# Performance work log

Hardware: AMD Instinct MI355X
Metric: run time of the kernel (lower is better)

Reference implementation:

```python
import jax, jax.numpy as jnp
import numpy as np

N_NODES = 50000


def _gcn_norm(edge_index, num_nodes):
    # PyG GCNConv default: add self-loops, symmetric normalization D^-1/2 A D^-1/2
    row, col = edge_index[0], edge_index[1]
    loop = jnp.arange(num_nodes, dtype=edge_index.dtype)
    row = jnp.concatenate([row, loop])
    col = jnp.concatenate([col, loop])
    deg = jax.ops.segment_sum(jnp.ones_like(col, dtype=jnp.float32), col,
                              num_segments=num_nodes)
    deg_inv_sqrt = jnp.where(deg > 0, jax.lax.rsqrt(deg), 0.0)
    norm = deg_inv_sqrt[row] * deg_inv_sqrt[col]  # [E + N]
    return row, col, norm


def _gcn_conv(x, row, col, norm, W, b):
    h = x @ W                                   # [N, out]
    msg = h[row] * norm[:, None]                # gather + scale, [E+N, out]
    out = jax.ops.segment_sum(msg, col, num_segments=x.shape[0])  # scatter-add
    return out + b


def setup_inputs() -> dict:
    key = jax.random.key(0)
    k_x, k_e, k_w1, k_w2 = jax.random.split(key, 4)
    n, e, d = N_NODES, 800000, 64
    x = jax.random.normal(k_x, (n, d), dtype=jnp.float32)
    edge_index = jax.random.randint(k_e, (2, e), 0, n, dtype=jnp.int64)
    # Glorot init like PyG's Linear inside GCNConv (bias separate, zero-init here as randn-small)
    s1 = (6.0 / (d + d)) ** 0.5
    W1 = jax.random.uniform(k_w1, (d, d), jnp.float32, -s1, s1)
    W2 = jax.random.uniform(k_w2, (d, d), jnp.float32, -s1, s1)
    b1 = jnp.zeros((d,), jnp.float32)
    b2 = jnp.zeros((d,), jnp.float32)
    return {"x": x, "edge_index": edge_index, "W1": W1, "b1": b1, "W2": W2, "b2": b2}


def reference(x, edge_index, W1, b1, W2, b2):
    row, col, norm = _gcn_norm(edge_index, x.shape[0])
    h = _gcn_conv(x, row, col, norm, W1, b1)   # layer 1: in -> out
    h = _gcn_conv(h, row, col, norm, W2, b2)   # layer 2: out -> out
    return h
```

## Files before the change

kernel.cpp:

```cpp
#include <hip/hip_runtime.h>
#include <hip/hip_fp16.h>

#define DD 64
#define BSH 6
#define BNODES 64
#define NSUB 16
#define SCAP 128
#define BCAP 1536

__global__ __launch_bounds__(256) void k_zero(int4* __restrict__ p, int n4) {
    int i = blockIdx.x * 256 + threadIdx.x;
    if (i < n4) p[i] = make_int4(0, 0, 0, 0);
}

__global__ __launch_bounds__(256) void k_fill3(const int* __restrict__ rowi,
                                               const int* __restrict__ coli,
                                               int* __restrict__ cur,
                                               unsigned int* __restrict__ pk, int E) {
    int i = blockIdx.x * 256 + threadIdx.x;
    if (i < E) {
        int c = coli[i];
        int idx = (c >> BSH) * NSUB + (blockIdx.x & (NSUB - 1));
        int p = atomicAdd(&cur[idx * 16], 1);
        if (p < SCAP)
            pk[(size_t)idx * SCAP + p] =
                (unsigned int)rowi[i] | ((unsigned int)(c & (BNODES - 1)) << 16);
    }
}

__global__ __launch_bounds__(256) void k_bsort(const int* __restrict__ cur,
                                               const unsigned int* __restrict__ pk,
                                               int* __restrict__ off_s,
                                               int* __restrict__ off_e,
                                               float* __restrict__ dis,
                                               int* __restrict__ srt, int n) {
    __shared__ unsigned int stage[NSUB * SCAP];
    __shared__ int cnt[BNODES];
    __shared__ int cbase[BNODES];
    __shared__ int sb[NSUB + 1];
    int t = threadIdx.x;
    int b = blockIdx.x;

    if (t < BNODES) cnt[t] = 0;
    if (t < NSUB) {
        int v = cur[(b * NSUB + t) * 16];
        if (v > SCAP) v = SCAP;
        int x = v;
#pragma unroll
        for (int d = 1; d < NSUB; d <<= 1) {
            int u = __shfl_up(x, d, NSUB);
            if ((t & (NSUB - 1)) >= d) x += u;
        }
        sb[t + 1] = x;
        if (t == 0) sb[0] = 0;
    }
    __syncthreads();
    int tot = sb[NSUB];

#pragma unroll
    for (int s = 0; s < NSUB; ++s) {
        int c0 = sb[s], len = sb[s + 1] - c0;
        const unsigned int* src = pk + ((size_t)b * NSUB + s) * SCAP;
        for (int i = t; i < len; i += 256) stage[c0 + i] = src[i];
    }
    __syncthreads();

    for (int i = t; i < tot; i += 256) atomicAdd(&cnt[stage[i] >> 16], 1);
    __syncthreads();

    if (t < BNODES) {
        int v = cnt[t], x = v;
#pragma unroll
        for (int d = 1; d < 64; d <<= 1) {
            int u = __shfl_up(x, d);
            if (t >= d) x += u;
        }
        int excl = x - v;
        cbase[t] = excl;
        int c = b * BNODES + t;
        if (c < n) {
            off_s[c] = b * BCAP + excl;
            off_e[c] = b * BCAP + excl + v;
            dis[c] = rsqrtf((float)(v + 1));
        }
    }
    __syncthreads();

    int sbeg = b * BCAP;
    for (int i = t; i < tot; i += 256) {
        unsigned int k = stage[i];
        int pos = atomicAdd(&cbase[k >> 16], 1);
        srt[sbeg + pos] = (int)(k & 0xFFFFu);
    }
}

__global__ __launch_bounds__(64) void k_mm(const float* __restrict__ X,
                                           const float* __restrict__ W,
                                           const float* __restrict__ dis,
                                           __half* __restrict__ H, int n) {
    int lane  = threadIdx.x;
    int tile  = blockIdx.x >> 1;
    int jbase = (blockIdx.x & 1) * 32;
    int r     = tile * 64 + lane;
    int rc    = min(r, n - 1);

    const float4* X4 = (const float4*)X;
    float acc[32];
#pragma unroll
    for (int j = 0; j < 32; ++j) acc[j] = 0.f;

#pragma unroll 1
    for (int kc = 0; kc < 16; ++kc) {
        float4 xv = X4[(size_t)rc * 16 + kc];
        const float* W0 = W + (kc * 4) * 64 + jbase;
#pragma unroll
        for (int u = 0; u < 4; ++u) {
            float xk = (u == 0) ? xv.x : (u == 1) ? xv.y : (u == 2) ? xv.z : xv.w;
            const float* Wk = W0 + u * 64;
#pragma unroll
            for (int j = 0; j < 32; ++j)
                acc[j] = fmaf(xk, Wk[j], acc[j]);
        }
    }
    if (r < n) {
        float d = dis[r];
        __half2 hh[16];
#pragma unroll
        for (int q = 0; q < 16; ++q)
            hh[q] = __floats2half2_rn(acc[2 * q] * d, acc[2 * q + 1] * d);
        uint4* dst = (uint4*)(H + (size_t)r * DD + jbase);
        const uint4* src = (const uint4*)hh;
#pragma unroll
        for (int q = 0; q < 4; ++q) dst[q] = src[q];
    }
}

__global__ __launch_bounds__(256) void k_agg(const int* __restrict__ off_s,
                                             const int* __restrict__ off_e,
                                             const int* __restrict__ srt,
                                             const float* __restrict__ dis,
                                             const __half* __restrict__ hs,
                                             const float* __restrict__ bias,
                                             float* __restrict__ out, int n, int totW) {
    int lane = threadIdx.x & 63;
    int j    = lane & 31;
    int hsel = lane >> 5;
    int wid  = __builtin_amdgcn_readfirstlane(blockIdx.x * 4 + (threadIdx.x >> 6));
    const __half2* hs2 = (const __half2*)hs;

    for (int c = wid; c < n; c += totW) {
        int s = __builtin_amdgcn_readfirstlane(off_s[c]);
        int e = __builtin_amdgcn_readfirstlane(off_e[c]);

        float ax = 0.f, ay = 0.f;
        if (hsel == 0) {
            float2 f = __half22float2(hs2[(size_t)c * 32 + j]);
            ax = f.x; ay = f.y;
        }
        int p = s;
        for (; p + 8 <= e; p += 8) {
            int r0 = srt[p + 0], r1 = srt[p + 1], r2 = srt[p + 2], r3 = srt[p + 3];
            int r4 = srt[p + 4], r5 = srt[p + 5], r6 = srt[p + 6], r7 = srt[p + 7];
            int ra = hsel ? r1 : r0;
            int rb = hsel ? r3 : r2;
            int rg = hsel ? r5 : r4;
            int rd = hsel ? r7 : r6;
            float2 f0 = __half22float2(hs2[(size_t)ra * 32 + j]);
            float2 f1 = __half22float2(hs2[(size_t)rb * 32 + j]);
            float2 f2 = __half22float2(hs2[(size_t)rg * 32 + j]);
            float2 f3 = __half22float2(hs2[(size_t)rd * 32 + j]);
            ax += (f0.x + f1.x) + (f2.x + f3.x);
            ay += (f0.y + f1.y) + (f2.y + f3.y);
        }
        for (; p + 2 <= e; p += 2) {
            int r0 = srt[p], r1 = srt[p + 1];
            int ra = hsel ? r1 : r0;
            float2 f = __half22float2(hs2[(size_t)ra * 32 + j]);
            ax += f.x; ay += f.y;
        }
        if (p < e && hsel == 0) {
            float2 f = __half22float2(hs2[(size_t)srt[p] * 32 + j]);
            ax += f.x; ay += f.y;
        }
        ax += __shfl_xor(ax, 32);
        ay += __shfl_xor(ay, 32);
        if (hsel == 0) {
            float d = dis[c];
            float2 bb = ((const float2*)bias)[j];
            ((float2*)out)[(size_t)c * 32 + j] = make_float2(bb.x + d * ax, bb.y + d * ay);
        }
    }
}

extern "C" void kernel_launch(void* const* d_in, const int* in_sizes, int n_in,
                              void* d_out, int out_size, void* d_ws, size_t ws_size,
                              hipStream_t stream) {
    const float* x  = (const float*)d_in[0];
    const int*   ei = (const int*)d_in[1];
    const float* W1 = (const float*)d_in[2];
    const float* b1 = (const float*)d_in[3];
    const float* W2 = (const float*)d_in[4];
    const float* b2 = (const float*)d_in[5];
    float* out = (float*)d_out;

    int n = in_sizes[0] / DD;
    int E = in_sizes[1] / 2;
    const int* rowi = ei;
    const int* coli = ei + E;
    int nb = (n + BNODES - 1) / BNODES;
    int M  = nb * NSUB;

    char* ws = (char*)d_ws;
    int*          cur   = (int*)ws;
    int*          off_s = (int*)(ws + (size_t)1024 * 1024);
    int*          off_e = (int*)(ws + (size_t)1280 * 1024);
    float*        dis   = (float*)(ws + (size_t)1536 * 1024);
    unsigned int* pk    = (unsigned int*)(ws + (size_t)2048 * 1024);
    int*          srt   = (int*)(ws + (size_t)8704 * 1024);
    __half*       hs    = (__half*)(ws + (size_t)14336 * 1024);
    float*        o1    = out;

    int n4    = M * 4;
    int nb_z  = (n4 + 255) / 256;
    int nb_e  = (E + 255) / 256;
    int nb_mm = ((n + 63) / 64) * 2;
    int nb_ag = 2048;
    int totW  = nb_ag * 4;

    k_zero <<<nb_z, 256, 0, stream>>>((int4*)cur, n4);
    k_fill3<<<nb_e, 256, 0, stream>>>(rowi, coli, cur, pk, E);
    k_bsort<<<nb, 256, 0, stream>>>(cur, pk, off_s, off_e, dis, srt, n);

    k_mm <<<nb_mm, 64, 0, stream>>>(x, W1, dis, hs, n);
    k_agg<<<nb_ag, 256, 0, stream>>>(off_s, off_e, srt, dis, hs, b1, o1, n, totW);

    k_mm <<<nb_mm, 64, 0, stream>>>(o1, W2, dis, hs, n);
    k_agg<<<nb_ag, 256, 0, stream>>>(off_s, off_e, srt, dis, hs, b2, out, n, totW);
}
```

Measured before the change: 132.8 us.

## Split feature halves into per-XCD arrays and shrink sorted indices to 16-bit

The transformed features are stored as two separate 32-column half-precision arrays, one per column half. The aggregation grid is split so that blocks on XCDs 0-3 handle one half and blocks on XCDs 4-7 handle the other. Each XCD's L2 therefore caches only a 3.2 MB half-table instead of the full table, and each wavefront gathers four neighbours at a time with 16 lanes per row. Sorted source indices are also narrowed from int to unsigned short to cut index traffic. This relies on the block-to-XCD round-robin mapping, doubles the per-node offset and degree reads, and adds an extra shuffle reduction.

```diff
diff --git a/kernel.cpp b/kernel.cpp
--- a/kernel.cpp
+++ b/kernel.cpp
@@ -33,7 +33,7 @@
                                                int* __restrict__ off_s,
                                                int* __restrict__ off_e,
                                                float* __restrict__ dis,
-                                               int* __restrict__ srt, int n) {
+                                               unsigned short* __restrict__ srt, int n) {
     __shared__ unsigned int stage[NSUB * SCAP];
     __shared__ int cnt[BNODES];
     __shared__ int cbase[BNODES];
@@ -90,14 +90,15 @@
     for (int i = t; i < tot; i += 256) {
         unsigned int k = stage[i];
         int pos = atomicAdd(&cbase[k >> 16], 1);
-        srt[sbeg + pos] = (int)(k & 0xFFFFu);
+        srt[sbeg + pos] = (unsigned short)(k & 0xFFFFu);
     }
 }
 
 __global__ __launch_bounds__(64) void k_mm(const float* __restrict__ X,
                                            const float* __restrict__ W,
                                            const float* __restrict__ dis,
-                                           __half* __restrict__ H, int n) {
+                                           __half* __restrict__ hsA,
+                                           __half* __restrict__ hsB, int n) {
     int lane  = threadIdx.x;
     int tile  = blockIdx.x >> 1;
     int jbase = (blockIdx.x & 1) * 32;
@@ -128,7 +129,8 @@
 #pragma unroll
         for (int q = 0; q < 16; ++q)
             hh[q] = __floats2half2_rn(acc[2 * q] * d, acc[2 * q + 1] * d);
-        uint4* dst = (uint4*)(H + (size_t)r * DD + jbase);
+        __half* Hrow = ((blockIdx.x & 1) ? hsB : hsA) + (size_t)r * 32;
+        uint4* dst = (uint4*)Hrow;
         const uint4* src = (const uint4*)hh;
 #pragma unroll
         for (int q = 0; q < 4; ++q) dst[q] = src[q];
@@ -137,16 +139,23 @@
 
 __global__ __launch_bounds__(256) void k_agg(const int* __restrict__ off_s,
                                              const int* __restrict__ off_e,
-                                             const int* __restrict__ srt,
+                                             const unsigned short* __restrict__ srt,
                                              const float* __restrict__ dis,
-                                             const __half* __restrict__ hs,
+                                             const __half* __restrict__ hsA,
+                                             const __half* __restrict__ hsB,
                                              const float* __restrict__ bias,
-                                             float* __restrict__ out, int n, int totW) {
-    int lane = threadIdx.x & 63;
-    int j    = lane & 31;
-    int hsel = lane >> 5;
-    int wid  = __builtin_amdgcn_readfirstlane(blockIdx.x * 4 + (threadIdx.x >> 6));
-    const __half2* hs2 = (const __half2*)hs;
+                                             float* __restrict__ out, int n) {
+    const int lane = threadIdx.x & 63;
+    const int j    = lane & 15;
+    const int hsel = lane >> 4;
+    const int xcd  = blockIdx.x & 7;
+    const int pass = xcd >> 2;
+    const int sub  = ((blockIdx.x >> 3) << 2) | (xcd & 3);
+    const int wid  = __builtin_amdgcn_readfirstlane(sub * 4 + ((threadIdx.x >> 6)));
+    const int totW = (gridDim.x >> 1) * 4;
+    const int fb   = pass << 5;
+
+    const __half2* hp = (const __half2*)(pass ? hsB : hsA);
 
     for (int c = wid; c < n; c += totW) {
         int s = __builtin_amdgcn_readfirstlane(off_s[c]);
@@ -154,40 +163,36 @@
 
         float ax = 0.f, ay = 0.f;
         if (hsel == 0) {
-            float2 f = __half22float2(hs2[(size_t)c * 32 + j]);
+            float2 f = __half22float2(hp[(size_t)c * 16 + j]);
             ax = f.x; ay = f.y;
         }
         int p = s;
         for (; p + 8 <= e; p += 8) {
-            int r0 = srt[p + 0], r1 = srt[p + 1], r2 = srt[p + 2], r3 = srt[p + 3];
-            int r4 = srt[p + 4], r5 = srt[p + 5], r6 = srt[p + 6], r7 = srt[p + 7];
-            int ra = hsel ? r1 : r0;
-            int rb = hsel ? r3 : r2;
-            int rg = hsel ? r5 : r4;
-            int rd = hsel ? r7 : r6;
-            float2 f0 = __half22float2(hs2[(size_t)ra * 32 + j]);
-            float2 f1 = __half22float2(hs2[(size_t)rb * 32 + j]);
-            float2 f2 = __half22float2(hs2[(size_t)rg * 32 + j]);
-            float2 f3 = __half22float2(hs2[(size_t)rd * 32 + j]);
-            ax += (f0.x + f1.x) + (f2.x + f3.x);
-            ay += (f0.y + f1.y) + (f2.y + f3.y);
-        }
-        for (; p + 2 <= e; p += 2) {
-            int r0 = srt[p], r1 = srt[p + 1];
-            int ra = hsel ? r1 : r0;
-            float2 f = __half22float2(hs2[(size_t)ra * 32 + j]);
-            ax += f.x; ay += f.y;
-        }
-        if (p < e && hsel == 0) {
-            float2 f = __half22float2(hs2[(size_t)srt[p] * 32 + j]);
-            ax += f.x; ay += f.y;
-        }
-        ax += __shfl_xor(ax, 32);
-        ay += __shfl_xor(ay, 32);
+            int ra = srt[p + hsel];
+            int rb = srt[p + 4 + hsel];
+            float2 fa = __half22float2(hp[(size_t)ra * 16 + j]);
+            float2 fc = __half22float2(hp[(size_t)rb * 16 + j]);
+            ax += fa.x + fc.x;
+            ay += fa.y + fc.y;
+        }
+        for (; p + 4 <= e; p += 4) {
+            int ra = srt[p + hsel];
+            float2 fa = __half22float2(hp[(size_t)ra * 16 + j]);
+            ax += fa.x; ay += fa.y;
+        }
+        int rem = e - p;
+        if (hsel < rem) {
+            int ra = srt[p + hsel];
+            float2 fa = __half22float2(hp[(size_t)ra * 16 + j]);
+            ax += fa.x; ay += fa.y;
+        }
+        ax += __shfl_xor(ax, 16); ay += __shfl_xor(ay, 16);
+        ax += __shfl_xor(ax, 32); ay += __shfl_xor(ay, 32);
         if (hsel == 0) {
             float d = dis[c];
-            float2 bb = ((const float2*)bias)[j];
-            ((float2*)out)[(size_t)c * 32 + j] = make_float2(bb.x + d * ax, bb.y + d * ay);
+            float2 bb = ((const float2*)(bias + fb))[j];
+            ((float2*)(out + (size_t)c * DD + fb))[j] =
+                make_float2(bb.x + d * ax, bb.y + d * ay);
         }
     }
 }
@@ -211,29 +216,29 @@
     int M  = nb * NSUB;
 
     char* ws = (char*)d_ws;
-    int*          cur   = (int*)ws;
-    int*          off_s = (int*)(ws + (size_t)1024 * 1024);
-    int*          off_e = (int*)(ws + (size_t)1280 * 1024);
-    float*        dis   = (float*)(ws + (size_t)1536 * 1024);
-    unsigned int* pk    = (unsigned int*)(ws + (size_t)2048 * 1024);
-    int*          srt   = (int*)(ws + (size_t)8704 * 1024);
-    __half*       hs    = (__half*)(ws + (size_t)14336 * 1024);
-    float*        o1    = out;
+    int*            cur   = (int*)ws;
+    int*            off_s = (int*)(ws + (size_t)1024 * 1024);
+    int*            off_e = (int*)(ws + (size_t)1280 * 1024);
+    float*          dis   = (float*)(ws + (size_t)1536 * 1024);
+    unsigned int*   pk    = (unsigned int*)(ws + (size_t)2048 * 1024);
+    unsigned short* srt   = (unsigned short*)(ws + (size_t)8704 * 1024);
+    __half*         hsA   = (__half*)(ws + (size_t)11776 * 1024);
+    __half*         hsB   = (__half*)(ws + (size_t)15360 * 1024);
+    float*          o1    = out;
 
     int n4    = M * 4;
     int nb_z  = (n4 + 255) / 256;
     int nb_e  = (E + 255) / 256;
     int nb_mm = ((n + 63) / 64) * 2;
     int nb_ag = 2048;
-    int totW  = nb_ag * 4;
 
     k_zero <<<nb_z, 256, 0, stream>>>((int4*)cur, n4);
     k_fill3<<<nb_e, 256, 0, stream>>>(rowi, coli, cur, pk, E);
     k_bsort<<<nb, 256, 0, stream>>>(cur, pk, off_s, off_e, dis, srt, n);
 
-    k_mm <<<nb_mm, 64, 0, stream>>>(x, W1, dis, hs, n);
-    k_agg<<<nb_ag, 256, 0, stream>>>(off_s, off_e, srt, dis, hs, b1, o1, n, totW);
-
-    k_mm <<<nb_mm, 64, 0, stream>>>(o1, W2, dis, hs, n);
-    k_agg<<<nb_ag, 256, 0, stream>>>(off_s, off_e, srt, dis, hs, b2, out, n, totW);
-}
+    k_mm <<<nb_mm, 64, 0, stream>>>(x, W1, dis, hsA, hsB, n);
+    k_agg<<<nb_ag, 256, 0, stream>>>(off_s, off_e, srt, dis, hsA, hsB, b1, o1, n);
+
+    k_mm <<<nb_mm, 64, 0, stream>>>(o1, W2, dis, hsA, hsB, n);
+    k_agg<<<nb_ag, 256, 0, stream>>>(off_s, off_e, srt, dis, hsA, hsB, b2, out, n);
+}
```

After: 157.2 us. 18.3% more time.
